# Performance work log

Hardware: AMD Instinct MI355X
Metric: run time of the kernel (lower is better)

The kernel has to match this reference:

```python
import jax, jax.numpy as jnp
import numpy as np

EPS = 1e-12  # F.normalize clamp_min


def setup_inputs() -> dict:
    key = jax.random.key(0)
    k1, k2, k3, k4 = jax.random.split(key, 4)
    emb_dim = 64
    user_feat = jax.random.normal(k1, (4096, emb_dim), dtype=jnp.float32)
    seq_feat = jax.random.normal(k2, (2048, 32, emb_dim), dtype=jnp.float32)
    # nn.Linear(emb_dim, emb_dim): weight [out, in], bias [out]
    bound = 1.0 / np.sqrt(emb_dim)
    W = jax.random.uniform(k3, (emb_dim, emb_dim), dtype=jnp.float32, minval=-bound, maxval=bound)
    b = jax.random.uniform(k4, (emb_dim,), dtype=jnp.float32, minval=-bound, maxval=bound)
    return {"user_feat": user_feat, "seq_feat": seq_feat, "W": W, "b": b}


def reference(user_feat, seq_feat, W, b):
    D = seq_feat.shape[-1]
    sf = seq_feat.reshape(-1, D)                       # [M, D]
    M = sf.shape[0]
    # attention scores + L1 row-normalization (F.normalize p=1, dim=1)
    att = jnp.einsum('nd,md->nm', user_feat, sf)       # [N, M]
    att = att / jnp.maximum(jnp.sum(jnp.abs(att), axis=1, keepdims=True), EPS)
    # mean_m Linear(att[n,m] * sf[m]) == (att @ sf)/M @ W^T + b  (affine distributivity)
    agg = jnp.einsum('nm,md->nd', att, sf) / M         # [N, D]
    message_mean = agg @ W.T + b                        # [N, D]
    return user_feat + message_mean
```

## Files before the change

### kernel.cpp

```cpp
#include <hip/hip_runtime.h>
#include <hip/hip_bf16.h>

typedef __attribute__((ext_vector_type(8))) short short8v;
typedef __attribute__((ext_vector_type(4))) float f32x4;

#define N_ROWS 4096
#define M_ROWS 65536
#define DIM 64

#define AS1C(p) ((const __attribute__((address_space(1))) void*)(p))
#define AS3(p)  ((__attribute__((address_space(3))) void*)(p))

__device__ inline unsigned short f2bf(float f) {
  unsigned u = __float_as_uint(f);
  unsigned r = (u + 0x7FFFu + ((u >> 16) & 1u)) >> 16;
  return (unsigned short)r;
}
__device__ inline float bf2f(unsigned short s) {
  return __uint_as_float(((unsigned)s) << 16);
}

__global__ __launch_bounds__(256) void cvt_kernel(const float* __restrict__ in,
                                                  unsigned short* __restrict__ out,
                                                  int n4) {
  int i = blockIdx.x * 256 + threadIdx.x;
  if (i >= n4) return;
  float4 v = reinterpret_cast<const float4*>(in)[i];
  ushort4 o;
  o.x = f2bf(v.x); o.y = f2bf(v.y); o.z = f2bf(v.z); o.w = f2bf(v.w);
  reinterpret_cast<ushort4*>(out)[i] = o;
}

__global__ __launch_bounds__(256) void s_kernel(const float* __restrict__ u,
                                                const unsigned short* __restrict__ sf16,
                                                float* __restrict__ Spart) {
  __shared__ unsigned short Bt[2][4096];
  const int bn = blockIdx.x;
  const int bm = blockIdx.y;
  const int tid = threadIdx.x;
  const int wid = tid >> 6;
  const int lane = tid & 63;
  const int l15 = lane & 15;
  const int lg  = lane >> 4;
  const int n0 = bn * 256 + wid * 64;
  const int mbase = bm * 1024;

  short8v au[4][2];
#pragma unroll
  for (int st = 0; st < 4; ++st) {
#pragma unroll
    for (int kf = 0; kf < 2; ++kf) {
      const float* ap = u + (size_t)(n0 + st * 16 + l15) * DIM + kf * 32 + lg * 8;
      float4 f0 = *reinterpret_cast<const float4*>(ap);
      float4 f1 = *reinterpret_cast<const float4*>(ap + 4);
      short8v v;
      v[0] = (short)f2bf(f0.x); v[1] = (short)f2bf(f0.y);
      v[2] = (short)f2bf(f0.z); v[3] = (short)f2bf(f0.w);
      v[4] = (short)f2bf(f1.x); v[5] = (short)f2bf(f1.y);
      v[6] = (short)f2bf(f1.z); v[7] = (short)f2bf(f1.w);
      au[st][kf] = v;
    }
  }

  f32x4 sacc[4];
#pragma unroll
  for (int st = 0; st < 4; ++st) sacc[st] = (f32x4){0.f, 0.f, 0.f, 0.f};

#define STAGE(buf, step)                                                       \
  {                                                                            \
    _Pragma("unroll") for (int j = 0; j < 2; ++j) {                            \
      const int kp = wid * 2 + j;                                              \
      const unsigned short* g =                                                \
          sf16 + (size_t)(mbase + (step) * 64 + lane) * DIM + kp * 8;          \
      __builtin_amdgcn_global_load_lds(AS1C(g), AS3(&Bt[buf][kp * 512]), 16, 0, 0); \
    }                                                                          \
  }

  STAGE(0, 0);
  for (int s = 0; s < 16; ++s) {
    __syncthreads();
    if (s < 15) STAGE((s + 1) & 1, s + 1);
    const unsigned short* B = &Bt[s & 1][0];
#pragma unroll
    for (int g = 0; g < 4; ++g) {
      short8v b0 = *reinterpret_cast<const short8v*>(
          &B[(size_t)lg * 512 + (g * 16 + l15) * 8]);
      short8v b1 = *reinterpret_cast<const short8v*>(
          &B[(size_t)(4 + lg) * 512 + (g * 16 + l15) * 8]);
#pragma unroll
      for (int st = 0; st < 4; ++st) {
        f32x4 acc = (f32x4){0.f, 0.f, 0.f, 0.f};
        acc = __builtin_amdgcn_mfma_f32_16x16x32_bf16(au[st][0], b0, acc, 0, 0, 0);
        acc = __builtin_amdgcn_mfma_f32_16x16x32_bf16(au[st][1], b1, acc, 0, 0, 0);
        sacc[st][0] += fabsf(acc[0]);
        sacc[st][1] += fabsf(acc[1]);
        sacc[st][2] += fabsf(acc[2]);
        sacc[st][3] += fabsf(acc[3]);
      }
    }
  }
#undef STAGE

#pragma unroll
  for (int off = 1; off < 16; off <<= 1) {
#pragma unroll
    for (int st = 0; st < 4; ++st) {
#pragma unroll
      for (int r = 0; r < 4; ++r)
        sacc[st][r] += __shfl_xor(sacc[st][r], off, 64);
    }
  }
  if (l15 == 0) {
#pragma unroll
    for (int st = 0; st < 4; ++st)
#pragma unroll
      for (int r = 0; r < 4; ++r)
        Spart[(size_t)(n0 + st * 16 + lg * 4 + r) * 64 + bm] = sacc[st][r];
  }
}

__global__ __launch_bounds__(512) void g_partial(const unsigned short* __restrict__ sf16,
                                                 float* __restrict__ Gp) {
  __shared__ unsigned short tile[128][DIM];
  const int tid = threadIdx.x;
  const int d1 = (tid & 15) * 4;
  const int d2 = (tid >> 4) * 2;
  float acc[4][2];
#pragma unroll
  for (int i = 0; i < 4; ++i)
#pragma unroll
    for (int j = 0; j < 2; ++j) acc[i][j] = 0.f;

  for (int ph = 0; ph < 2; ++ph) {
    {
      const int r = tid >> 2, q = tid & 3;
      const short8v* src = reinterpret_cast<const short8v*>(
          sf16 + (size_t)(blockIdx.x * 256 + ph * 128 + r) * DIM + q * 16);
      short8v* dst = reinterpret_cast<short8v*>(&tile[r][q * 16]);
      dst[0] = src[0];
      dst[1] = src[1];
    }
    __syncthreads();
#pragma unroll 8
    for (int m = 0; m < 128; ++m) {
      ushort4 a4 = *reinterpret_cast<const ushort4*>(&tile[m][d1]);
      ushort2 b2 = *reinterpret_cast<const ushort2*>(&tile[m][d2]);
      float a[4] = {bf2f(a4.x), bf2f(a4.y), bf2f(a4.z), bf2f(a4.w)};
      float b[2] = {bf2f(b2.x), bf2f(b2.y)};
#pragma unroll
      for (int i = 0; i < 4; ++i)
#pragma unroll
        for (int j = 0; j < 2; ++j) acc[i][j] += a[i] * b[j];
    }
    __syncthreads();
  }
#pragma unroll
  for (int i = 0; i < 4; ++i)
#pragma unroll
    for (int j = 0; j < 2; ++j)
      Gp[(size_t)blockIdx.x * 4096 + (d1 + i) * DIM + (d2 + j)] = acc[i][j];
}

__global__ __launch_bounds__(256) void gp_reduce_p(const float* __restrict__ Gp,
                                                   const float* __restrict__ W,
                                                   float* __restrict__ P) {
  const int j = blockIdx.x;
  const int d = threadIdx.x & 63;
  const int q = threadIdx.x >> 6;
  float g = 0.f;
#pragma unroll 8
  for (int i = 0; i < 64; ++i)
    g += Gp[(size_t)(q + 4 * i) * 4096 + j * DIM + d];
  __shared__ float part[4][DIM];
  part[q][d] = g;
  __syncthreads();
  if (q == 0) {
    float row = part[0][d] + part[1][d] + part[2][d] + part[3][d];
    part[0][d] = row;
  }
  __syncthreads();
  if (q == 0) {
    float acc = 0.f;
#pragma unroll
    for (int k = 0; k < DIM; ++k) acc += part[0][k] * W[d * DIM + k];
    P[j * DIM + d] = acc;
  }
}

__global__ __launch_bounds__(256) void out_kernel(const float* __restrict__ u,
                                                  const float* __restrict__ P,
                                                  const float* __restrict__ Spart,
                                                  const float* __restrict__ bias,
                                                  float* __restrict__ out) {
  __shared__ float Ps[DIM][DIM];
  __shared__ float us[4][DIM];
  const int tid = threadIdx.x;
#pragma unroll
  for (int i = 0; i < 16; ++i)
    (&Ps[0][0])[tid + i * 256] = P[tid + i * 256];
  const int base = blockIdx.x * 256;
  us[tid >> 6][tid & 63] = u[base + tid];
  __syncthreads();

  const int nl = tid >> 6;
  const int d = tid & 63;
  const int n = blockIdx.x * 4 + nl;

  float sp = Spart[(size_t)n * 64 + d];
#pragma unroll
  for (int off = 1; off < 64; off <<= 1) sp += __shfl_xor(sp, off, 64);
  const float inv = 1.f / (fmaxf(sp, 1e-12f) * (float)M_ROWS);

  float acc = 0.f;
#pragma unroll
  for (int jj = 0; jj < DIM; ++jj) acc += us[nl][jj] * Ps[jj][d];
  out[base + tid] = us[nl][d] + acc * inv + bias[d];
}

extern "C" void kernel_launch(void* const* d_in, const int* in_sizes, int n_in,
                              void* d_out, int out_size, void* d_ws, size_t ws_size,
                              hipStream_t stream) {
  const float* u  = (const float*)d_in[0];
  const float* sf = (const float*)d_in[1];
  const float* W  = (const float*)d_in[2];
  const float* b  = (const float*)d_in[3];
  float* out = (float*)d_out;

  char* ws = (char*)d_ws;
  unsigned short* sf16 = (unsigned short*)ws;
  float* Spart = (float*)(ws + 8388608);
  float* Gp    = (float*)(ws + 9437184);
  float* P     = (float*)(ws + 13631488);

  cvt_kernel<<<dim3(M_ROWS * DIM / 4 / 256), 256, 0, stream>>>(sf, sf16, M_ROWS * DIM / 4);
  s_kernel<<<dim3(16, 64), 256, 0, stream>>>(u, sf16, Spart);
  g_partial<<<dim3(256), 512, 0, stream>>>(sf16, Gp);
  gp_reduce_p<<<dim3(64), 256, 0, stream>>>(Gp, W, P);
  out_kernel<<<dim3(N_ROWS * 64 / 256), 256, 0, stream>>>(u, P, Spart, b, out);
}
```

Measured before the change: 135.6 us.

## Fuse bf16 conversion with Gram partials and enlarge s_kernel tiles

The fp32-to-bf16 conversion of seq_feat is merged with the Gram-matrix partial computation, so each block converts 128 rows, writes them out and reuses them from LDS to build a partial sf^T sf. This removes a separate kernel launch and a re-read of sf16. The s_kernel tile is doubled to 512 user rows per block, with each wave holding 8 A subtiles and a 128-row B stage. That halves the grid to 8x64 blocks and raises register and LDS use per block. gp_reduce_p now sums 512 partials instead of 256, and P is moved to a new workspace offset to fit the larger Gp buffer.

```diff
diff --git a/kernel.cpp b/kernel.cpp
--- a/kernel.cpp
+++ b/kernel.cpp
@@ -20,21 +20,54 @@
   return __uint_as_float(((unsigned)s) << 16);
 }
 
-__global__ __launch_bounds__(256) void cvt_kernel(const float* __restrict__ in,
-                                                  unsigned short* __restrict__ out,
-                                                  int n4) {
-  int i = blockIdx.x * 256 + threadIdx.x;
-  if (i >= n4) return;
-  float4 v = reinterpret_cast<const float4*>(in)[i];
-  ushort4 o;
-  o.x = f2bf(v.x); o.y = f2bf(v.y); o.z = f2bf(v.z); o.w = f2bf(v.w);
-  reinterpret_cast<ushort4*>(out)[i] = o;
+__global__ __launch_bounds__(256) void cvt_g_kernel(const float* __restrict__ sf,
+                                                    unsigned short* __restrict__ sf16,
+                                                    float* __restrict__ Gp) {
+  __shared__ unsigned short tile[128 * DIM];
+  const int tid = threadIdx.x;
+  const size_t base = (size_t)blockIdx.x * 128 * DIM;
+
+#pragma unroll
+  for (int j = 0; j < 8; ++j) {
+    const int e = tid * 4 + j * 1024;
+    float4 v = *reinterpret_cast<const float4*>(sf + base + e);
+    ushort4 o;
+    o.x = f2bf(v.x); o.y = f2bf(v.y); o.z = f2bf(v.z); o.w = f2bf(v.w);
+    *reinterpret_cast<ushort4*>(sf16 + base + e) = o;
+    *reinterpret_cast<ushort4*>(&tile[e]) = o;
+  }
+  __syncthreads();
+
+  const int d1 = (tid & 15) * 4;
+  const int d2 = (tid >> 4) * 4;
+  float acc[4][4];
+#pragma unroll
+  for (int i = 0; i < 4; ++i)
+#pragma unroll
+    for (int j = 0; j < 4; ++j) acc[i][j] = 0.f;
+
+#pragma unroll 8
+  for (int m = 0; m < 128; ++m) {
+    ushort4 a4 = *reinterpret_cast<const ushort4*>(&tile[m * DIM + d1]);
+    ushort4 b4 = *reinterpret_cast<const ushort4*>(&tile[m * DIM + d2]);
+    float a[4] = {bf2f(a4.x), bf2f(a4.y), bf2f(a4.z), bf2f(a4.w)};
+    float b[4] = {bf2f(b4.x), bf2f(b4.y), bf2f(b4.z), bf2f(b4.w)};
+#pragma unroll
+    for (int i = 0; i < 4; ++i)
+#pragma unroll
+      for (int j = 0; j < 4; ++j) acc[i][j] += a[i] * b[j];
+  }
+#pragma unroll
+  for (int i = 0; i < 4; ++i)
+#pragma unroll
+    for (int j = 0; j < 4; ++j)
+      Gp[(size_t)blockIdx.x * 4096 + (d1 + i) * DIM + (d2 + j)] = acc[i][j];
 }
 
 __global__ __launch_bounds__(256) void s_kernel(const float* __restrict__ u,
                                                 const unsigned short* __restrict__ sf16,
                                                 float* __restrict__ Spart) {
-  __shared__ unsigned short Bt[2][4096];
+  __shared__ unsigned short Bt[2][8192];
   const int bn = blockIdx.x;
   const int bm = blockIdx.y;
   const int tid = threadIdx.x;
@@ -42,12 +75,12 @@
   const int lane = tid & 63;
   const int l15 = lane & 15;
   const int lg  = lane >> 4;
-  const int n0 = bn * 256 + wid * 64;
+  const int n0 = bn * 512 + wid * 128;
   const int mbase = bm * 1024;
 
-  short8v au[4][2];
-#pragma unroll
-  for (int st = 0; st < 4; ++st) {
+  short8v au[8][2];
+#pragma unroll
+  for (int st = 0; st < 8; ++st) {
 #pragma unroll
     for (int kf = 0; kf < 2; ++kf) {
       const float* ap = u + (size_t)(n0 + st * 16 + l15) * DIM + kf * 32 + lg * 8;
@@ -62,33 +95,35 @@
     }
   }
 
-  f32x4 sacc[4];
-#pragma unroll
-  for (int st = 0; st < 4; ++st) sacc[st] = (f32x4){0.f, 0.f, 0.f, 0.f};
+  f32x4 sacc[8];
+#pragma unroll
+  for (int st = 0; st < 8; ++st) sacc[st] = (f32x4){0.f, 0.f, 0.f, 0.f};
 
 #define STAGE(buf, step)                                                       \
   {                                                                            \
-    _Pragma("unroll") for (int j = 0; j < 2; ++j) {                            \
-      const int kp = wid * 2 + j;                                              \
+    _Pragma("unroll") for (int j = 0; j < 4; ++j) {                            \
+      const int idx = wid * 4 + j;                                             \
+      const int kp = idx >> 1;                                                 \
+      const int h = idx & 1;                                                   \
       const unsigned short* g =                                                \
-          sf16 + (size_t)(mbase + (step) * 64 + lane) * DIM + kp * 8;          \
-      __builtin_amdgcn_global_load_lds(AS1C(g), AS3(&Bt[buf][kp * 512]), 16, 0, 0); \
+          sf16 + (size_t)(mbase + (step) * 128 + h * 64 + lane) * DIM + kp * 8;\
+      __builtin_amdgcn_global_load_lds(AS1C(g), AS3(&Bt[buf][kp * 1024 + h * 512]), 16, 0, 0); \
     }                                                                          \
   }
 
   STAGE(0, 0);
-  for (int s = 0; s < 16; ++s) {
+  for (int s = 0; s < 8; ++s) {
     __syncthreads();
-    if (s < 15) STAGE((s + 1) & 1, s + 1);
+    if (s < 7) STAGE((s + 1) & 1, s + 1);
     const unsigned short* B = &Bt[s & 1][0];
 #pragma unroll
-    for (int g = 0; g < 4; ++g) {
+    for (int g = 0; g < 8; ++g) {
       short8v b0 = *reinterpret_cast<const short8v*>(
-          &B[(size_t)lg * 512 + (g * 16 + l15) * 8]);
+          &B[(size_t)lg * 1024 + (g * 16 + l15) * 8]);
       short8v b1 = *reinterpret_cast<const short8v*>(
-          &B[(size_t)(4 + lg) * 512 + (g * 16 + l15) * 8]);
-#pragma unroll
-      for (int st = 0; st < 4; ++st) {
+          &B[(size_t)(4 + lg) * 1024 + (g * 16 + l15) * 8]);
+#pragma unroll
+      for (int st = 0; st < 8; ++st) {
         f32x4 acc = (f32x4){0.f, 0.f, 0.f, 0.f};
         acc = __builtin_amdgcn_mfma_f32_16x16x32_bf16(au[st][0], b0, acc, 0, 0, 0);
         acc = __builtin_amdgcn_mfma_f32_16x16x32_bf16(au[st][1], b1, acc, 0, 0, 0);
@@ -104,7 +139,7 @@
 #pragma unroll
   for (int off = 1; off < 16; off <<= 1) {
 #pragma unroll
-    for (int st = 0; st < 4; ++st) {
+    for (int st = 0; st < 8; ++st) {
 #pragma unroll
       for (int r = 0; r < 4; ++r)
         sacc[st][r] += __shfl_xor(sacc[st][r], off, 64);
@@ -112,53 +147,11 @@
   }
   if (l15 == 0) {
 #pragma unroll
-    for (int st = 0; st < 4; ++st)
+    for (int st = 0; st < 8; ++st)
 #pragma unroll
       for (int r = 0; r < 4; ++r)
         Spart[(size_t)(n0 + st * 16 + lg * 4 + r) * 64 + bm] = sacc[st][r];
   }
-}
-
-__global__ __launch_bounds__(512) void g_partial(const unsigned short* __restrict__ sf16,
-                                                 float* __restrict__ Gp) {
-  __shared__ unsigned short tile[128][DIM];
-  const int tid = threadIdx.x;
-  const int d1 = (tid & 15) * 4;
-  const int d2 = (tid >> 4) * 2;
-  float acc[4][2];
-#pragma unroll
-  for (int i = 0; i < 4; ++i)
-#pragma unroll
-    for (int j = 0; j < 2; ++j) acc[i][j] = 0.f;
-
-  for (int ph = 0; ph < 2; ++ph) {
-    {
-      const int r = tid >> 2, q = tid & 3;
-      const short8v* src = reinterpret_cast<const short8v*>(
-          sf16 + (size_t)(blockIdx.x * 256 + ph * 128 + r) * DIM + q * 16);
-      short8v* dst = reinterpret_cast<short8v*>(&tile[r][q * 16]);
-      dst[0] = src[0];
-      dst[1] = src[1];
-    }
-    __syncthreads();
-#pragma unroll 8
-    for (int m = 0; m < 128; ++m) {
-      ushort4 a4 = *reinterpret_cast<const ushort4*>(&tile[m][d1]);
-      ushort2 b2 = *reinterpret_cast<const ushort2*>(&tile[m][d2]);
-      float a[4] = {bf2f(a4.x), bf2f(a4.y), bf2f(a4.z), bf2f(a4.w)};
-      float b[2] = {bf2f(b2.x), bf2f(b2.y)};
-#pragma unroll
-      for (int i = 0; i < 4; ++i)
-#pragma unroll
-        for (int j = 0; j < 2; ++j) acc[i][j] += a[i] * b[j];
-    }
-    __syncthreads();
-  }
-#pragma unroll
-  for (int i = 0; i < 4; ++i)
-#pragma unroll
-    for (int j = 0; j < 2; ++j)
-      Gp[(size_t)blockIdx.x * 4096 + (d1 + i) * DIM + (d2 + j)] = acc[i][j];
 }
 
 __global__ __launch_bounds__(256) void gp_reduce_p(const float* __restrict__ Gp,
@@ -169,7 +162,7 @@
   const int q = threadIdx.x >> 6;
   float g = 0.f;
 #pragma unroll 8
-  for (int i = 0; i < 64; ++i)
+  for (int i = 0; i < 128; ++i)
     g += Gp[(size_t)(q + 4 * i) * 4096 + j * DIM + d];
   __shared__ float part[4][DIM];
   part[q][d] = g;
@@ -230,11 +223,10 @@
   unsigned short* sf16 = (unsigned short*)ws;
   float* Spart = (float*)(ws + 8388608);
   float* Gp    = (float*)(ws + 9437184);
-  float* P     = (float*)(ws + 13631488);
-
-  cvt_kernel<<<dim3(M_ROWS * DIM / 4 / 256), 256, 0, stream>>>(sf, sf16, M_ROWS * DIM / 4);
-  s_kernel<<<dim3(16, 64), 256, 0, stream>>>(u, sf16, Spart);
-  g_partial<<<dim3(256), 512, 0, stream>>>(sf16, Gp);
+  float* P     = (float*)(ws + 17825792);
+
+  cvt_g_kernel<<<dim3(512), 256, 0, stream>>>(sf, sf16, Gp);
+  s_kernel<<<dim3(8, 64), 256, 0, stream>>>(u, sf16, Spart);
   gp_reduce_p<<<dim3(64), 256, 0, stream>>>(Gp, W, P);
   out_kernel<<<dim3(N_ROWS * 64 / 256), 256, 0, stream>>>(u, P, Spart, b, out);
 }
```

After: 148.4 us. +9.4%, slower.
